# Kernel optimization log

Hardware: AMD Instinct MI355X
Metric: run time of the kernel (lower is better)

The kernel has to match this reference:

```python
import jax, jax.numpy as jnp
import numpy as np

B, N, D = 16384, 64, 64

def setup_inputs() -> dict:
    key = jax.random.key(0)
    ks = jax.random.split(key, 8)
    return {
        "self_vectors": jax.random.normal(ks[0], (B, 1, D), dtype=jnp.float32),
        "neighbor_vectors": jax.random.normal(ks[1], (B, 1, N, D), dtype=jnp.float32),
        "neighbor_relations": jax.random.normal(ks[2], (B, 1, N, D), dtype=jnp.float32),
        "user_embeddings": jax.random.normal(ks[3], (B, D), dtype=jnp.float32),
        "W1": jax.random.normal(ks[4], (2 * D, D), dtype=jnp.float32) * (1.0 / np.sqrt(2 * D)),
        "b1": jnp.zeros((D,), dtype=jnp.float32),
        "w2": jax.random.normal(ks[5], (D, 1), dtype=jnp.float32) * (1.0 / np.sqrt(D)),
        "b2": jnp.zeros((1,), dtype=jnp.float32),
    }

def reference(self_vectors, neighbor_vectors, neighbor_relations, user_embeddings, W1, b1, w2, b2):
    b, _, n, d = neighbor_relations.shape
    # user embedding broadcast over neighbors: [b,1,n,d]
    ue = jnp.broadcast_to(user_embeddings[:, None, None, :], (b, 1, n, d))
    head_rel = jnp.concatenate([ue, neighbor_relations], axis=-1)  # [b,1,n,2d]
    hidden = jax.nn.relu(head_rel @ W1 + b1)                        # [b,1,n,d]
    decay = jax.nn.sigmoid(hidden @ w2 + b2)                        # [b,1,n,1]
    decay = jax.nn.softmax(decay, axis=2)                           # softmax over neighbors
    agg = jnp.sum(decay * neighbor_vectors, axis=2)                 # [b,1,d]
    return jnp.concatenate([self_vectors, agg], axis=-1)           # [b,1,2d]
```

## Files before the change

### kernel.cpp

```cpp
#include <hip/hip_runtime.h>
#include <math.h>

#define BATCH 16384
#define NN 64
#define DD 64
#define RS 65

__global__ __launch_bounds__(256, 8)
void aggregator_kernel(const float* __restrict__ self_v,
                       const float* __restrict__ nv,
                       const float* __restrict__ rel,
                       const float* __restrict__ ue,
                       const float* __restrict__ W1,
                       const float* __restrict__ b1,
                       const float* __restrict__ w2,
                       const float* __restrict__ b2,
                       float* __restrict__ out)
{
    const int b = blockIdx.x;
    const int t = threadIdx.x;
    const int lane = t & 63;
    const int w = __builtin_amdgcn_readfirstlane(t >> 6);

    __shared__ float rel_s[NN * RS];
    __shared__ float red_s[4][DD];
    __shared__ float agg_s[4][DD];

    const float* __restrict__ relb = rel + (size_t)b * (NN * DD);

    #pragma unroll
    for (int i = 0; i < 4; ++i) {
        int idx = i * 256 + t;
        float4 v = ((const float4*)relb)[idx];
        int n = idx >> 4;
        int k = (idx & 15) * 4;
        float* p = &rel_s[n * RS + k];
        p[0] = v.x; p[1] = v.y; p[2] = v.z; p[3] = v.w;
    }

    {
        const float* __restrict__ ueb = ue + (size_t)b * DD + 16 * w;
        float pu = 0.0f;
        #pragma unroll
        for (int kk = 0; kk < 16; ++kk) {
            pu = fmaf(ueb[kk], W1[(16 * w + kk) * DD + lane], pu);
        }
        red_s[w][lane] = pu;
    }
    __syncthreads();

    float acc[16];
    {
        const float* __restrict__ b1q = b1 + 16 * w;
        #pragma unroll
        for (int jj = 0; jj < 16; ++jj) {
            int j = 16 * w + jj;
            acc[jj] = b1q[jj] + red_s[0][j] + red_s[1][j] + red_s[2][j] + red_s[3][j];
        }
    }

    const float* __restrict__ Wq = W1 + DD * DD + 16 * w;
    #pragma unroll 4
    for (int k = 0; k < DD; ++k) {
        float x = rel_s[lane * RS + k];
        const float* __restrict__ row = Wq + (size_t)k * DD;
        #pragma unroll
        for (int jj = 0; jj < 16; ++jj) acc[jj] = fmaf(x, row[jj], acc[jj]);
    }

    {
        const float* __restrict__ w2q = w2 + 16 * w;
        float pd = 0.0f;
        #pragma unroll
        for (int jj = 0; jj < 16; ++jj) pd = fmaf(fmaxf(acc[jj], 0.0f), w2q[jj], pd);
        __syncthreads();
        red_s[w][lane] = pd;
    }
    __syncthreads();

    float d = b2[0] + red_s[0][lane] + red_s[1][lane] + red_s[2][lane] + red_s[3][lane];
    float dec = 1.0f / (1.0f + __expf(-d));
    float m = dec;
    #pragma unroll
    for (int off = 32; off > 0; off >>= 1) m = fmaxf(m, __shfl_xor(m, off, 64));
    float e = __expf(dec - m);
    float s = e;
    #pragma unroll
    for (int off = 32; off > 0; off >>= 1) s += __shfl_xor(s, off, 64);
    float wv = e / s;

    const float* __restrict__ nvb = nv + (size_t)b * (NN * DD) + (size_t)(16 * w) * DD + lane;
    float pa = 0.0f;
    #pragma unroll
    for (int i = 0; i < 16; ++i) {
        float wi = __shfl(wv, 16 * w + i, 64);
        pa = fmaf(wi, nvb[(size_t)i * DD], pa);
    }
    agg_s[w][lane] = pa;
    __syncthreads();

    if (t < 64) {
        out[(size_t)b * (2 * DD) + t] = self_v[(size_t)b * DD + t];
    } else if (t < 128) {
        int j = t - 64;
        out[(size_t)b * (2 * DD) + DD + j] =
            agg_s[0][j] + agg_s[1][j] + agg_s[2][j] + agg_s[3][j];
    }
}

extern "C" void kernel_launch(void* const* d_in, const int* in_sizes, int n_in,
                              void* d_out, int out_size, void* d_ws, size_t ws_size,
                              hipStream_t stream) {
    const float* self_v = (const float*)d_in[0];
    const float* nv     = (const float*)d_in[1];
    const float* rel    = (const float*)d_in[2];
    const float* ue     = (const float*)d_in[3];
    const float* W1     = (const float*)d_in[4];
    const float* b1     = (const float*)d_in[5];
    const float* w2     = (const float*)d_in[6];
    const float* b2     = (const float*)d_in[7];
    float* out = (float*)d_out;

    aggregator_kernel<<<dim3(BATCH), dim3(256), 0, stream>>>(
        self_v, nv, rel, ue, W1, b1, w2, b2, out);
}
```

Measured before the change: 533.2 us.

## Prefetch neighbor vectors and rel rows into registers, drop extra barrier

Rel tiles are loaded into registers before the user-embedding projection and written to LDS afterward. The neighbor-vector loads are issued right after the first barrier so they overlap the hidden-layer matmul. A separate pd_s buffer removes one __syncthreads, and the self-vector copy is loaded early. The cost is higher register pressure (16 extra floats plus four float4 registers) under launch_bounds(256,8), which could cause spills or lower occupancy.

```diff
diff --git a/kernel.cpp b/kernel.cpp
--- a/kernel.cpp
+++ b/kernel.cpp
@@ -23,20 +23,15 @@
     const int w = __builtin_amdgcn_readfirstlane(t >> 6);
 
     __shared__ float rel_s[NN * RS];
-    __shared__ float red_s[4][DD];
+    __shared__ float u1p_s[4][DD];
+    __shared__ float pd_s[4][DD];
     __shared__ float agg_s[4][DD];
 
     const float* __restrict__ relb = rel + (size_t)b * (NN * DD);
 
+    float4 r[4];
     #pragma unroll
-    for (int i = 0; i < 4; ++i) {
-        int idx = i * 256 + t;
-        float4 v = ((const float4*)relb)[idx];
-        int n = idx >> 4;
-        int k = (idx & 15) * 4;
-        float* p = &rel_s[n * RS + k];
-        p[0] = v.x; p[1] = v.y; p[2] = v.z; p[3] = v.w;
-    }
+    for (int i = 0; i < 4; ++i) r[i] = ((const float4*)relb)[i * 256 + t];
 
     {
         const float* __restrict__ ueb = ue + (size_t)b * DD + 16 * w;
@@ -45,18 +40,32 @@
         for (int kk = 0; kk < 16; ++kk) {
             pu = fmaf(ueb[kk], W1[(16 * w + kk) * DD + lane], pu);
         }
-        red_s[w][lane] = pu;
+        u1p_s[w][lane] = pu;
+    }
+
+    float sv = 0.0f;
+    if (w == 0) sv = self_v[(size_t)b * DD + lane];
+
+    #pragma unroll
+    for (int i = 0; i < 4; ++i) {
+        int idx = i * 256 + t;
+        int n = idx >> 4;
+        int k = (idx & 15) * 4;
+        float* p = &rel_s[n * RS + k];
+        p[0] = r[i].x; p[1] = r[i].y; p[2] = r[i].z; p[3] = r[i].w;
     }
     __syncthreads();
 
+    const float* __restrict__ nvb = nv + (size_t)b * (NN * DD) + (size_t)(16 * w) * DD + lane;
+    float nvr[16];
+    #pragma unroll
+    for (int i = 0; i < 16; ++i) nvr[i] = nvb[(size_t)i * DD];
+
     float acc[16];
-    {
-        const float* __restrict__ b1q = b1 + 16 * w;
-        #pragma unroll
-        for (int jj = 0; jj < 16; ++jj) {
-            int j = 16 * w + jj;
-            acc[jj] = b1q[jj] + red_s[0][j] + red_s[1][j] + red_s[2][j] + red_s[3][j];
-        }
+    #pragma unroll
+    for (int jj = 0; jj < 16; ++jj) {
+        int j = 16 * w + jj;
+        acc[jj] = b1[j] + u1p_s[0][j] + u1p_s[1][j] + u1p_s[2][j] + u1p_s[3][j];
     }
 
     const float* __restrict__ Wq = W1 + DD * DD + 16 * w;
@@ -73,12 +82,11 @@
         float pd = 0.0f;
         #pragma unroll
         for (int jj = 0; jj < 16; ++jj) pd = fmaf(fmaxf(acc[jj], 0.0f), w2q[jj], pd);
-        __syncthreads();
-        red_s[w][lane] = pd;
+        pd_s[w][lane] = pd;
     }
     __syncthreads();
 
-    float d = b2[0] + red_s[0][lane] + red_s[1][lane] + red_s[2][lane] + red_s[3][lane];
+    float d = b2[0] + pd_s[0][lane] + pd_s[1][lane] + pd_s[2][lane] + pd_s[3][lane];
     float dec = 1.0f / (1.0f + __expf(-d));
     float m = dec;
     #pragma unroll
@@ -89,22 +97,20 @@
     for (int off = 32; off > 0; off >>= 1) s += __shfl_xor(s, off, 64);
     float wv = e / s;
 
-    const float* __restrict__ nvb = nv + (size_t)b * (NN * DD) + (size_t)(16 * w) * DD + lane;
     float pa = 0.0f;
     #pragma unroll
     for (int i = 0; i < 16; ++i) {
         float wi = __shfl(wv, 16 * w + i, 64);
-        pa = fmaf(wi, nvb[(size_t)i * DD], pa);
+        pa = fmaf(wi, nvr[i], pa);
     }
     agg_s[w][lane] = pa;
+
+    if (w == 0) out[(size_t)b * (2 * DD) + lane] = sv;
     __syncthreads();
 
-    if (t < 64) {
-        out[(size_t)b * (2 * DD) + t] = self_v[(size_t)b * DD + t];
-    } else if (t < 128) {
-        int j = t - 64;
-        out[(size_t)b * (2 * DD) + DD + j] =
-            agg_s[0][j] + agg_s[1][j] + agg_s[2][j] + agg_s[3][j];
+    if (w == 0) {
+        out[(size_t)b * (2 * DD) + DD + lane] =
+            agg_s[0][lane] + agg_s[1][lane] + agg_s[2][lane] + agg_s[3][lane];
     }
 }
 
```

New measurement: 533.0 us. About the same (-0.1%).
